# Optimization experiments

Hardware: AMD Instinct MI355X
Metric: run time of the kernel (lower is better)

Reference implementation:

```python
import jax, jax.numpy as jnp
import numpy as np

CONF_THRES = 0.8
NMS_THRES = 0.4
MAX_DET = 300          # fixed capacity for jit-compatible NMS output
N_BOXES = 262144
N_CLASSES = 80


def xywh2xyxy(x):
    xy, wh = x[..., :2], x[..., 2:4]
    return jnp.concatenate([xy - wh * 0.5, xy + wh * 0.5], axis=-1)


def bbox_iou(box, boxes):
    # one box [4] vs many [N,4]; original uses the +1 pixel-area convention
    x1 = jnp.maximum(box[0], boxes[:, 0])
    y1 = jnp.maximum(box[1], boxes[:, 1])
    x2 = jnp.minimum(box[2], boxes[:, 2])
    y2 = jnp.minimum(box[3], boxes[:, 3])
    inter = jnp.clip(x2 - x1 + 1, 0) * jnp.clip(y2 - y1 + 1, 0)
    a1 = (box[2] - box[0] + 1) * (box[3] - box[1] + 1)
    a2 = (boxes[:, 2] - boxes[:, 0] + 1) * (boxes[:, 3] - boxes[:, 1] + 1)
    return inter / (a1 + a2 - inter + 1e-16)


def nms_single(pred):
    # pred: [N, 85] raw YOLO output for one image
    boxes = xywh2xyxy(pred[:, :4])
    obj = pred[:, 4]
    cls_scores = pred[:, 5:]
    class_conf = cls_scores.max(axis=-1)
    class_pred = jnp.argmax(cls_scores, axis=-1).astype(pred.dtype)
    valid = obj >= CONF_THRES
    score = obj * class_conf
    # sort valid boxes by descending score; invalid pushed to the end
    order = jnp.argsort(jnp.where(valid, -score, jnp.inf))
    det = jnp.concatenate(
        [boxes, obj[:, None], class_conf[:, None], class_pred[:, None]], axis=1
    )[order]  # [N, 7] = x1,y1,x2,y2,obj,class_conf,class_pred
    valid = valid[order]

    def step(valid, _):
        idx = jnp.argmax(valid)            # first still-valid (= highest score)
        any_valid = jnp.any(valid)
        cur = det[idx]
        iou = bbox_iou(cur[:4], det[:, :4])
        invalid = (iou > NMS_THRES) & (det[:, 6] == cur[6]) & valid
        # weighted box merge over the suppressed group (as in original NMS)
        w = jnp.where(invalid, det[:, 4], 0.0)
        merged = (w[:, None] * det[:, :4]).sum(0) / (w.sum() + 1e-16)
        out = jnp.where(any_valid,
                        jnp.concatenate([merged, cur[4:]]),
                        jnp.zeros(7, pred.dtype))
        return valid & ~invalid, (out, any_valid)

    _, (kept, kept_valid) = jax.lax.scan(step, valid, None, length=MAX_DET)
    return kept, kept_valid  # [MAX_DET,7], [MAX_DET]


def setup_inputs() -> dict:
    key = jax.random.key(0)
    detections = jax.random.uniform(key, (1, N_BOXES, 5 + N_CLASSES), dtype=jnp.float32)
    return {"detections": detections}


def reference(detections):
    kept, kv = nms_single(detections[0])
    d = kept[:, 5:]                        # [MAX_DET, 2] = (class_conf, class_pred)
    conf_key = jnp.where(kv, d[:, 0], -jnp.inf)  # padded rows sort to the end
    order = jnp.argsort(conf_key)          # ascending (torch argsort)
    d = d[order][::-1]                     # torch.flip -> descending class_conf
    kv = kv[order][::-1]
    probs = jnp.where(kv, d[:, 0], 0.0)    # self.probs
    ids = d[:, 1][None, :]                 # self.ids, shape [1, MAX_DET]
    return ids, probs
```

## Files before the change

### kernel.cpp

```cpp
#include <hip/hip_runtime.h>

#pragma clang fp contract(off)

#define NBOX 262144
#define NCLS 80
#define ROWS 85
#define CAP 1024
#define NSUB 8
#define SUBCAP 128
#define POOL 8192
#define BPT 2
#define S1BOX 512

typedef unsigned long long ull;

__global__ __launch_bounds__(1024) void k_init(int* __restrict__ cnt_pad,
                                               int* __restrict__ pool_count,
                                               int* __restrict__ done_count) {
    const int t = threadIdx.x;
    for (int i = t; i < NCLS * NSUB * 16; i += 1024) cnt_pad[i] = 0;
    if (t == 0) { *pool_count = 0; *done_count = 0; }
}

__global__ __launch_bounds__(256) void k_stage1(const float* __restrict__ det,
                                                int* __restrict__ cnt_pad,
                                                ull* __restrict__ key2,
                                                float* __restrict__ conf2,
                                                float4* __restrict__ box2) {
    __shared__ int s_wl[S1BOX];
    __shared__ float s_obj[S1BOX];
    __shared__ int s_nv;
    const int t = threadIdx.x;
    const int b0 = blockIdx.x * S1BOX;
    const int sb = blockIdx.x & (NSUB - 1);

    if (t == 0) s_nv = 0;
    __syncthreads();

    float obj[BPT];
    #pragma unroll
    for (int i = 0; i < BPT; i++)
        obj[i] = det[(size_t)(b0 + (i << 8) + t) * ROWS + 4];
    #pragma unroll
    for (int i = 0; i < BPT; i++) {
        if (obj[i] >= 0.8f) {
            int r = atomicAdd(&s_nv, 1);
            s_wl[r] = (i << 8) + t;
            s_obj[r] = obj[i];
        }
    }
    __syncthreads();
    const int nv = s_nv;

    const int grp = t >> 4, c = t & 15;
    const int lane = t & 63;
    #pragma unroll 2
    for (int r0 = 0; r0 < nv; r0 += 16) {
        int widx = r0 + grp;
        if (widx < nv) {
            int b = s_wl[widx];
            const float* p = det + (size_t)(b0 + b) * ROWS;
            float aux = (c < 5) ? p[c] : 0.0f;
            float v0 = p[5 + c];
            float v1 = p[21 + c];
            float v2 = p[37 + c];
            float v3 = p[53 + c];
            float v4 = p[69 + c];
            float mv = v0; int mj = c;
            if (v1 > mv) { mv = v1; mj = 16 + c; }
            if (v2 > mv) { mv = v2; mj = 32 + c; }
            if (v3 > mv) { mv = v3; mj = 48 + c; }
            if (v4 > mv) { mv = v4; mj = 64 + c; }
            #pragma unroll
            for (int off = 8; off; off >>= 1) {
                float ov = __shfl_xor(mv, off);
                int oj = __shfl_xor(mj, off);
                if (ov > mv || (ov == mv && oj < mj)) { mv = ov; mj = oj; }
            }
            int gb = lane & 48;
            float x = __shfl(aux, gb + 0);
            float y = __shfl(aux, gb + 1);
            float w = __shfl(aux, gb + 2);
            float h = __shfl(aux, gb + 3);
            if (c == 0) {
                float ob = s_obj[widx];
                float score = ob * mv;
                float hw = w * 0.5f, hh = h * 0.5f;
                int gi = b0 + b;
                int r = atomicAdd(&cnt_pad[((mj * NSUB + sb) << 4)], 1);
                if (r < SUBCAP) {
                    int pos = (mj << 10) + (sb << 7) + r;
                    key2[pos] = ((ull)(~__float_as_uint(score)) << 32) | (unsigned)gi;
                    conf2[pos] = mv;
                    box2[pos] = make_float4(x - hw, y - hh, x + hw, y + hh);
                }
            }
        }
    }
}

__device__ __forceinline__ void bsort512(ull (&x)[8], int lane) {
    #pragma unroll
    for (int k = 2; k <= 512; k <<= 1) {
        #pragma unroll
        for (int j = k >> 1; j >= 64; j >>= 1) {
            const int jr = j >> 6;
            #pragma unroll
            for (int r2 = 0; r2 < 8; r2++) {
                if ((r2 & jr) == 0) {
                    const bool asc = (((r2 << 6) & k) == 0);
                    ull a = x[r2], b = x[r2 | jr];
                    if ((a > b) == asc) { x[r2] = b; x[r2 | jr] = a; }
                }
            }
        }
        #pragma unroll
        for (int j = ((k >> 1) > 32 ? 32 : (k >> 1)); j >= 1; j >>= 1) {
            #pragma unroll
            for (int r2 = 0; r2 < 8; r2++) {
                int i = (r2 << 6) + lane;
                bool asc = ((i & k) == 0);
                ull o = __shfl_xor(x[r2], j);
                bool lower = ((lane & j) == 0);
                ull mn = x[r2] < o ? x[r2] : o;
                ull mx2 = x[r2] < o ? o : x[r2];
                x[r2] = (asc == lower) ? mn : mx2;
            }
        }
    }
}

__global__ __launch_bounds__(256) void k_nmsfinal(const int* __restrict__ cnt_pad,
                                                  const ull* __restrict__ key2,
                                                  const float* __restrict__ conf2,
                                                  const float4* __restrict__ box2,
                                                  ull* __restrict__ pool_key,
                                                  float* __restrict__ pool_conf,
                                                  int* __restrict__ pool_cls,
                                                  int* __restrict__ pool_count,
                                                  int* __restrict__ done_count,
                                                  float* __restrict__ out) {
    __shared__ int s_cnt[NSUB];
    __shared__ ull s_wkey[4];
    __shared__ float s_wbox[4][6];
    __shared__ int s_base;
    __shared__ int s_fin;
    __shared__ ull pkey[304];
    __shared__ float pconf[304];
    __shared__ int s_hist[256];
    __shared__ int s_wt[4];
    __shared__ int s_stat[4];
    __shared__ ull s_buf[512];
    __shared__ unsigned s_cb[512];
    __shared__ unsigned s_cl[512];

    const int c = blockIdx.x, t = threadIdx.x, lane = t & 63, wave = t >> 6;
    const int s0 = c << 10;

    ull k4[4]; float x1[4], y1[4], x2[4], y2[4], ar[4], cf[4];
    #pragma unroll
    for (int j = 0; j < 4; j++) {
        int pos = (wave << 8) + (j << 6) + lane;
        k4[j] = key2[s0 + pos];
        float4 b = box2[s0 + pos];
        x1[j] = b.x; y1[j] = b.y; x2[j] = b.z; y2[j] = b.w;
        cf[j] = conf2[s0 + pos];
    }
    if (t < NSUB) s_cnt[t] = min(cnt_pad[((c * NSUB + t) << 4)], SUBCAP);
    __syncthreads();
    #pragma unroll
    for (int j = 0; j < 4; j++) {
        int pos = (wave << 8) + (j << 6) + lane;
        bool ok = (pos & (SUBCAP - 1)) < s_cnt[pos >> 7];
        if (!ok) {
            k4[j] = ~0ULL;
            x1[j] = 0.f; y1[j] = 0.f; x2[j] = 0.f; y2[j] = 0.f; cf[j] = 0.f;
        }
        ar[j] = (x2[j] - x1[j] + 1.0f) * (y2[j] - y1[j] + 1.0f);
    }

    int np = 0;
    while (np < 300) {
        ull va = k4[0]; int ia = 0;
        if (k4[1] < va) { va = k4[1]; ia = 1; }
        ull vb = k4[2]; int ib = 2;
        if (k4[3] < vb) { vb = k4[3]; ib = 3; }
        ull lm = va; int lj = ia;
        if (vb < va) { lm = vb; lj = ib; }
        unsigned lo = (unsigned)lm;
        unsigned hi = (unsigned)(lm >> 32);
        unsigned mh = hi;
        #pragma unroll
        for (int off = 32; off; off >>= 1) {
            unsigned o = __shfl_xor(mh, off);
            mh = o < mh ? o : mh;
        }
        ull wb = __ballot(hi == mh);
        ull wm; int wl;
        if (__popcll(wb) != 1) {
            ull g = (hi == mh) ? lm : ~0ULL;
            #pragma unroll
            for (int off = 32; off; off >>= 1) {
                ull o = __shfl_xor(g, off);
                if (o < g) g = o;
            }
            wm = g;
            wb = __ballot(lm == wm);
            wl = (int)__ffsll((long long)wb) - 1;
        } else {
            wl = (int)__ffsll((long long)wb) - 1;
            wm = ((ull)mh << 32) | (ull)__shfl(lo, wl);
        }
        if (lane == wl) {
            s_wkey[wave] = wm;
            s_wbox[wave][0] = x1[lj]; s_wbox[wave][1] = y1[lj];
            s_wbox[wave][2] = x2[lj]; s_wbox[wave][3] = y2[lj];
            s_wbox[wave][4] = ar[lj]; s_wbox[wave][5] = cf[lj];
        }
        __syncthreads();
        ull gk = s_wkey[0]; int gw = 0;
        #pragma unroll
        for (int w2 = 1; w2 < 4; w2++) {
            ull kk = s_wkey[w2];
            if (kk < gk) { gk = kk; gw = w2; }
        }
        if (gk == ~0ULL) break;
        float cx1 = s_wbox[gw][0], cy1 = s_wbox[gw][1];
        float cx2 = s_wbox[gw][2], cy2 = s_wbox[gw][3];
        float a1 = s_wbox[gw][4];
        if (t == 0) { pkey[np] = gk; pconf[np] = s_wbox[gw][5]; }
        np++;
        #pragma unroll
        for (int j = 0; j < 4; j++) {
            float xx1 = fmaxf(cx1, x1[j]), yy1 = fmaxf(cy1, y1[j]);
            float xx2 = fminf(cx2, x2[j]), yy2 = fminf(cy2, y2[j]);
            float iw = xx2 - xx1 + 1.0f, ih = yy2 - yy1 + 1.0f;
            float inter = fmaxf(iw, 0.0f) * fmaxf(ih, 0.0f);
            float iou = inter / (a1 + ar[j] - inter + 1e-16f);
            if (iou > 0.4f) k4[j] = ~0ULL;
        }
        __syncthreads();
    }

    const int npw = np;
    if (t == 0 && npw) s_base = atomicAdd(pool_count, npw);
    __syncthreads();
    for (int j = t; j < npw; j += 256) {
        int pp = s_base + j;
        if (pp < POOL) {
            ull gm = pkey[j];
            ull pk = ((ull)((unsigned)(gm >> 32) & 0x7FFFFFFFu) << 32)
                   | ((gm & 0xFFFFFFFFull) << 14) | (ull)pp;
            __hip_atomic_store(&pool_key[pp], pk,
                               __ATOMIC_RELAXED, __HIP_MEMORY_SCOPE_AGENT);
            __hip_atomic_store(&pool_conf[pp], pconf[j],
                               __ATOMIC_RELAXED, __HIP_MEMORY_SCOPE_AGENT);
            __hip_atomic_store(&pool_cls[pp], c,
                               __ATOMIC_RELAXED, __HIP_MEMORY_SCOPE_AGENT);
        }
    }
    asm volatile("s_waitcnt vmcnt(0)" ::: "memory");
    __syncthreads();
    if (t == 0) {
        int ticket = atomicAdd(done_count, 1);
        s_fin = (ticket == NCLS - 1) ? 1 : 0;
    }
    __syncthreads();
    if (!s_fin) return;

    const int K = min(__hip_atomic_load(pool_count, __ATOMIC_RELAXED,
                                        __HIP_MEMORY_SCOPE_AGENT), POOL);
    ull key[32];
    #pragma unroll
    for (int j = 0; j < 32; j++) {
        int pos = t + (j << 8);
        key[j] = (pos < K) ? __hip_atomic_load(&pool_key[pos], __ATOMIC_RELAXED,
                                               __HIP_MEMORY_SCOPE_AGENT)
                           : ~0ULL;
    }

    const bool selAll = (K <= 511);
    int sh = 55;
    ull pfin = 0;
    if (!selAll) {
        ull p = 0;
        int gBelow = 0, r = 300;
        while (true) {
            s_hist[t] = 0;
            __syncthreads();
            #pragma unroll
            for (int j = 0; j < 32; j++) {
                ull kk = key[j];
                if ((kk >> (sh + 8)) == p)
                    atomicAdd(&s_hist[(int)((kk >> sh) & 0xFFull)], 1);
            }
            __syncthreads();
            int v = s_hist[t];
            int incv = v;
            for (int off = 1; off < 64; off <<= 1) {
                int o = __shfl_up(incv, off);
                if (lane >= off) incv += o;
            }
            if (lane == 63) s_wt[wave] = incv;
            __syncthreads();
            int wo = 0;
            #pragma unroll
            for (int w2 = 0; w2 < 4; w2++) if (w2 < wave) wo += s_wt[w2];
            int cumIncl = wo + incv;
            int cumExcl = cumIncl - v;
            if (cumExcl < r && r <= cumIncl) {
                s_stat[0] = t; s_stat[1] = cumExcl; s_stat[2] = cumIncl;
            }
            __syncthreads();
            int D = s_stat[0], below = s_stat[1], incl = s_stat[2];
            if (gBelow + incl <= 511 || sh == 7) {
                pfin = (p << 8) | (ull)D;
                break;
            }
            p = (p << 8) | (ull)D;
            gBelow += below;
            r = 300 - gBelow;
            sh -= 8;
            __syncthreads();
        }
    }

    if (t == 0) s_stat[3] = 0;
    __syncthreads();
    int ci = 0;
    #pragma unroll
    for (int j = 0; j < 32; j++) {
        ull kk = key[j];
        bool sel = selAll ? ((kk >> 63) == 0) : ((kk >> sh) <= pfin);
        if (sel) ci++;
    }
    int inc = ci;
    for (int off = 1; off < 64; off <<= 1) {
        int o = __shfl_up(inc, off);
        if (lane >= off) inc += o;
    }
    int wtot = __shfl(inc, 63);
    int wbase2 = 0;
    if (lane == 0 && wtot) wbase2 = atomicAdd(&s_stat[3], wtot);
    wbase2 = __shfl(wbase2, 0);
    int wp = wbase2 + inc - ci;
    #pragma unroll
    for (int j = 0; j < 32; j++) {
        ull kk = key[j];
        bool sel = selAll ? ((kk >> 63) == 0) : ((kk >> sh) <= pfin);
        if (sel) s_buf[wp++] = kk;
    }
    __syncthreads();
    const int S = s_stat[3];
    for (int i = t; i < 512; i += 256) if (i >= S) s_buf[i] = ~0ULL;
    __syncthreads();
    if (wave != 0) return;

    #pragma clang loop unroll(disable)
    for (int pass = 0; pass < 2; pass++) {
        ull x[8];
        #pragma unroll
        for (int r2 = 0; r2 < 8; r2++) x[r2] = s_buf[(r2 << 6) + lane];
        bsort512(x, lane);
        if (pass == 0) {
            #pragma unroll
            for (int r2 = 0; r2 < 8; r2++) {
                int i = (r2 << 6) + lane;
                ull kk = x[r2];
                ull k2 = ~0ULL;
                if (i < 300 && kk != ~0ULL) {
                    int pidx = (int)(kk & 0x3FFFull);
                    unsigned cb = __float_as_uint(
                        __hip_atomic_load(&pool_conf[pidx], __ATOMIC_RELAXED,
                                          __HIP_MEMORY_SCOPE_AGENT));
                    unsigned cl = (unsigned)__hip_atomic_load(&pool_cls[pidx],
                                          __ATOMIC_RELAXED, __HIP_MEMORY_SCOPE_AGENT);
                    s_cb[i] = cb; s_cl[i] = cl;
                    k2 = ((ull)(~cb) << 32) | (unsigned)(~i);
                }
                s_buf[i] = k2;
            }
        } else {
            #pragma unroll
            for (int r2 = 0; r2 < 8; r2++) {
                int i = (r2 << 6) + lane;
                if (i < 300) {
                    ull kk = x[r2];
                    float idv = 0.0f, pv = 0.0f;
                    if (kk != ~0ULL) {
                        int slot = (int)(~(unsigned)(kk & 0xFFFFFFFFull));
                        pv = __uint_as_float(s_cb[slot]);
                        idv = (float)(int)s_cl[slot];
                    }
                    out[i] = idv;
                    out[300 + i] = pv;
                }
            }
        }
    }
}

extern "C" void kernel_launch(void* const* d_in, const int* in_sizes, int n_in,
                              void* d_out, int out_size, void* d_ws, size_t ws_size,
                              hipStream_t stream) {
    const float* det = (const float*)d_in[0];
    float* out = (float*)d_out;
    char* ws = (char*)d_ws;

    int* cnt_pad = (int*)(ws + 0);
    int* pool_count = (int*)(ws + 40960);
    int* done_count = (int*)(ws + 40964);
    ull* key2 = (ull*)(ws + 41024);
    float* conf2 = (float*)(ws + 696384);
    float4* box2 = (float4*)(ws + 1024064);
    ull* pool_key = (ull*)(ws + 2334784);
    float* pool_conf = (float*)(ws + 2400320);
    int* pool_cls = (int*)(ws + 2433088);

    k_init<<<1, 1024, 0, stream>>>(cnt_pad, pool_count, done_count);
    k_stage1<<<NBOX / S1BOX, 256, 0, stream>>>(det, cnt_pad, key2, conf2, box2);
    k_nmsfinal<<<NCLS, 256, 0, stream>>>(cnt_pad, key2, conf2, box2,
                                         pool_key, pool_conf, pool_cls, pool_count,
                                         done_count, out);
}
```

Baseline: 170.8 us.

## Fuse stage1 and per-class NMS into one persistent kernel with grid barriers

Merges the filtering/argmax stage and the per-class NMS plus final selection into a single kernel of 256 blocks. Spin-wait grid barriers on a global counter replace the kernel boundaries, and the last-block ticket is swapped for a second barrier where block 0 runs the final merge. Stage1 now handles 1024 boxes per block instead of 512, so the grid drops from 512 to 256 blocks. The aim is to remove launch gaps between kernels, at the cost of requiring all 256 blocks to be co-resident, atomic stores and loads in place of plain ones, and a bounded spin that could race if the guard expires.

```diff
diff --git a/kernel.cpp b/kernel.cpp
--- a/kernel.cpp
+++ b/kernel.cpp
@@ -9,10 +9,14 @@
 #define NSUB 8
 #define SUBCAP 128
 #define POOL 8192
-#define BPT 2
-#define S1BOX 512
+#define NBLK 256
+#define S1PB 1024
 
 typedef unsigned long long ull;
+
+__device__ __forceinline__ ull packf2(float a, float b) {
+    return ((ull)__float_as_uint(b) << 32) | (ull)__float_as_uint(a);
+}
 
 __global__ __launch_bounds__(1024) void k_init(int* __restrict__ cnt_pad,
                                                int* __restrict__ pool_count,
@@ -22,81 +26,17 @@
     if (t == 0) { *pool_count = 0; *done_count = 0; }
 }
 
-__global__ __launch_bounds__(256) void k_stage1(const float* __restrict__ det,
-                                                int* __restrict__ cnt_pad,
-                                                ull* __restrict__ key2,
-                                                float* __restrict__ conf2,
-                                                float4* __restrict__ box2) {
-    __shared__ int s_wl[S1BOX];
-    __shared__ float s_obj[S1BOX];
-    __shared__ int s_nv;
-    const int t = threadIdx.x;
-    const int b0 = blockIdx.x * S1BOX;
-    const int sb = blockIdx.x & (NSUB - 1);
-
-    if (t == 0) s_nv = 0;
+__device__ __forceinline__ void gsync(int* done, int target, int t) {
     __syncthreads();
-
-    float obj[BPT];
-    #pragma unroll
-    for (int i = 0; i < BPT; i++)
-        obj[i] = det[(size_t)(b0 + (i << 8) + t) * ROWS + 4];
-    #pragma unroll
-    for (int i = 0; i < BPT; i++) {
-        if (obj[i] >= 0.8f) {
-            int r = atomicAdd(&s_nv, 1);
-            s_wl[r] = (i << 8) + t;
-            s_obj[r] = obj[i];
-        }
+    if (t == 0) {
+        __hip_atomic_fetch_add(done, 1, __ATOMIC_RELAXED, __HIP_MEMORY_SCOPE_AGENT);
+        int guard = 0;
+        while (__hip_atomic_load(done, __ATOMIC_RELAXED,
+                                 __HIP_MEMORY_SCOPE_AGENT) < target &&
+               ++guard < (1 << 18))
+            __builtin_amdgcn_s_sleep(8);
     }
     __syncthreads();
-    const int nv = s_nv;
-
-    const int grp = t >> 4, c = t & 15;
-    const int lane = t & 63;
-    #pragma unroll 2
-    for (int r0 = 0; r0 < nv; r0 += 16) {
-        int widx = r0 + grp;
-        if (widx < nv) {
-            int b = s_wl[widx];
-            const float* p = det + (size_t)(b0 + b) * ROWS;
-            float aux = (c < 5) ? p[c] : 0.0f;
-            float v0 = p[5 + c];
-            float v1 = p[21 + c];
-            float v2 = p[37 + c];
-            float v3 = p[53 + c];
-            float v4 = p[69 + c];
-            float mv = v0; int mj = c;
-            if (v1 > mv) { mv = v1; mj = 16 + c; }
-            if (v2 > mv) { mv = v2; mj = 32 + c; }
-            if (v3 > mv) { mv = v3; mj = 48 + c; }
-            if (v4 > mv) { mv = v4; mj = 64 + c; }
-            #pragma unroll
-            for (int off = 8; off; off >>= 1) {
-                float ov = __shfl_xor(mv, off);
-                int oj = __shfl_xor(mj, off);
-                if (ov > mv || (ov == mv && oj < mj)) { mv = ov; mj = oj; }
-            }
-            int gb = lane & 48;
-            float x = __shfl(aux, gb + 0);
-            float y = __shfl(aux, gb + 1);
-            float w = __shfl(aux, gb + 2);
-            float h = __shfl(aux, gb + 3);
-            if (c == 0) {
-                float ob = s_obj[widx];
-                float score = ob * mv;
-                float hw = w * 0.5f, hh = h * 0.5f;
-                int gi = b0 + b;
-                int r = atomicAdd(&cnt_pad[((mj * NSUB + sb) << 4)], 1);
-                if (r < SUBCAP) {
-                    int pos = (mj << 10) + (sb << 7) + r;
-                    key2[pos] = ((ull)(~__float_as_uint(score)) << 32) | (unsigned)gi;
-                    conf2[pos] = mv;
-                    box2[pos] = make_float4(x - hw, y - hh, x + hw, y + hh);
-                }
-            }
-        }
-    }
 }
 
 __device__ __forceinline__ void bsort512(ull (&x)[8], int lane) {
@@ -130,21 +70,24 @@
     }
 }
 
-__global__ __launch_bounds__(256) void k_nmsfinal(const int* __restrict__ cnt_pad,
-                                                  const ull* __restrict__ key2,
-                                                  const float* __restrict__ conf2,
-                                                  const float4* __restrict__ box2,
-                                                  ull* __restrict__ pool_key,
-                                                  float* __restrict__ pool_conf,
-                                                  int* __restrict__ pool_cls,
-                                                  int* __restrict__ pool_count,
-                                                  int* __restrict__ done_count,
-                                                  float* __restrict__ out) {
+__global__ __launch_bounds__(256) void k_mega(const float* __restrict__ det,
+                                              int* __restrict__ cnt_pad,
+                                              ull* __restrict__ key2,
+                                              float* __restrict__ conf2,
+                                              float4* __restrict__ box2,
+                                              ull* __restrict__ pool_key,
+                                              float* __restrict__ pool_conf,
+                                              int* __restrict__ pool_cls,
+                                              int* __restrict__ pool_count,
+                                              int* __restrict__ done_count,
+                                              float* __restrict__ out) {
+    __shared__ int s_wl[S1PB];
+    __shared__ float s_obj[S1PB];
+    __shared__ int s_nv;
     __shared__ int s_cnt[NSUB];
     __shared__ ull s_wkey[4];
     __shared__ float s_wbox[4][6];
     __shared__ int s_base;
-    __shared__ int s_fin;
     __shared__ ull pkey[304];
     __shared__ float pconf[304];
     __shared__ int s_hist[256];
@@ -154,119 +97,204 @@
     __shared__ unsigned s_cb[512];
     __shared__ unsigned s_cl[512];
 
-    const int c = blockIdx.x, t = threadIdx.x, lane = t & 63, wave = t >> 6;
-    const int s0 = c << 10;
-
-    ull k4[4]; float x1[4], y1[4], x2[4], y2[4], ar[4], cf[4];
-    #pragma unroll
-    for (int j = 0; j < 4; j++) {
-        int pos = (wave << 8) + (j << 6) + lane;
-        k4[j] = key2[s0 + pos];
-        float4 b = box2[s0 + pos];
-        x1[j] = b.x; y1[j] = b.y; x2[j] = b.z; y2[j] = b.w;
-        cf[j] = conf2[s0 + pos];
-    }
-    if (t < NSUB) s_cnt[t] = min(cnt_pad[((c * NSUB + t) << 4)], SUBCAP);
-    __syncthreads();
-    #pragma unroll
-    for (int j = 0; j < 4; j++) {
-        int pos = (wave << 8) + (j << 6) + lane;
-        bool ok = (pos & (SUBCAP - 1)) < s_cnt[pos >> 7];
-        if (!ok) {
-            k4[j] = ~0ULL;
-            x1[j] = 0.f; y1[j] = 0.f; x2[j] = 0.f; y2[j] = 0.f; cf[j] = 0.f;
-        }
-        ar[j] = (x2[j] - x1[j] + 1.0f) * (y2[j] - y1[j] + 1.0f);
-    }
-
-    int np = 0;
-    while (np < 300) {
-        ull va = k4[0]; int ia = 0;
-        if (k4[1] < va) { va = k4[1]; ia = 1; }
-        ull vb = k4[2]; int ib = 2;
-        if (k4[3] < vb) { vb = k4[3]; ib = 3; }
-        ull lm = va; int lj = ia;
-        if (vb < va) { lm = vb; lj = ib; }
-        unsigned lo = (unsigned)lm;
-        unsigned hi = (unsigned)(lm >> 32);
-        unsigned mh = hi;
-        #pragma unroll
-        for (int off = 32; off; off >>= 1) {
-            unsigned o = __shfl_xor(mh, off);
-            mh = o < mh ? o : mh;
-        }
-        ull wb = __ballot(hi == mh);
-        ull wm; int wl;
-        if (__popcll(wb) != 1) {
-            ull g = (hi == mh) ? lm : ~0ULL;
+    const int bid = blockIdx.x, t = threadIdx.x, lane = t & 63, wave = t >> 6;
+
+    {
+        const int b0 = bid << 10;
+        const int sb = bid & (NSUB - 1);
+        if (t == 0) s_nv = 0;
+        __syncthreads();
+        float obj[4];
+        #pragma unroll
+        for (int i = 0; i < 4; i++)
+            obj[i] = det[(size_t)(b0 + (i << 8) + t) * ROWS + 4];
+        #pragma unroll
+        for (int i = 0; i < 4; i++) {
+            if (obj[i] >= 0.8f) {
+                int r = atomicAdd(&s_nv, 1);
+                s_wl[r] = (i << 8) + t;
+                s_obj[r] = obj[i];
+            }
+        }
+        __syncthreads();
+        const int nv = s_nv;
+
+        const int grp = t >> 4, c = t & 15;
+        #pragma unroll 2
+        for (int r0 = 0; r0 < nv; r0 += 16) {
+            int widx = r0 + grp;
+            if (widx < nv) {
+                int b = s_wl[widx];
+                const float* p = det + (size_t)(b0 + b) * ROWS;
+                float aux = (c < 5) ? p[c] : 0.0f;
+                float v0 = p[5 + c];
+                float v1 = p[21 + c];
+                float v2 = p[37 + c];
+                float v3 = p[53 + c];
+                float v4 = p[69 + c];
+                float mv = v0; int mj = c;
+                if (v1 > mv) { mv = v1; mj = 16 + c; }
+                if (v2 > mv) { mv = v2; mj = 32 + c; }
+                if (v3 > mv) { mv = v3; mj = 48 + c; }
+                if (v4 > mv) { mv = v4; mj = 64 + c; }
+                #pragma unroll
+                for (int off = 8; off; off >>= 1) {
+                    float ov = __shfl_xor(mv, off);
+                    int oj = __shfl_xor(mj, off);
+                    if (ov > mv || (ov == mv && oj < mj)) { mv = ov; mj = oj; }
+                }
+                int gb = lane & 48;
+                float x = __shfl(aux, gb + 0);
+                float y = __shfl(aux, gb + 1);
+                float w = __shfl(aux, gb + 2);
+                float h = __shfl(aux, gb + 3);
+                if (c == 0) {
+                    float ob = s_obj[widx];
+                    float score = ob * mv;
+                    float hw = w * 0.5f, hh = h * 0.5f;
+                    int gi = b0 + b;
+                    int r = atomicAdd(&cnt_pad[((mj * NSUB + sb) << 4)], 1);
+                    if (r < SUBCAP) {
+                        int pos = (mj << 10) + (sb << 7) + r;
+                        __hip_atomic_store(&key2[pos],
+                            ((ull)(~__float_as_uint(score)) << 32) | (unsigned)gi,
+                            __ATOMIC_RELAXED, __HIP_MEMORY_SCOPE_AGENT);
+                        __hip_atomic_store(&conf2[pos], mv,
+                            __ATOMIC_RELAXED, __HIP_MEMORY_SCOPE_AGENT);
+                        ull* bp = (ull*)&box2[pos];
+                        __hip_atomic_store(bp + 0, packf2(x - hw, y - hh),
+                            __ATOMIC_RELAXED, __HIP_MEMORY_SCOPE_AGENT);
+                        __hip_atomic_store(bp + 1, packf2(x + hw, y + hh),
+                            __ATOMIC_RELAXED, __HIP_MEMORY_SCOPE_AGENT);
+                    }
+                }
+            }
+        }
+    }
+
+    gsync(done_count, NBLK, t);
+
+    if (bid < NCLS) {
+        const int c = bid;
+        const int s0 = c << 10;
+        ull k4[4]; float x1[4], y1[4], x2[4], y2[4], ar[4], cf[4];
+        #pragma unroll
+        for (int j = 0; j < 4; j++) {
+            int pos = s0 + (wave << 8) + (j << 6) + lane;
+            k4[j] = __hip_atomic_load(&key2[pos], __ATOMIC_RELAXED,
+                                      __HIP_MEMORY_SCOPE_AGENT);
+            ull* bp = (ull*)&box2[pos];
+            ull blo = __hip_atomic_load(bp + 0, __ATOMIC_RELAXED,
+                                        __HIP_MEMORY_SCOPE_AGENT);
+            ull bhi = __hip_atomic_load(bp + 1, __ATOMIC_RELAXED,
+                                        __HIP_MEMORY_SCOPE_AGENT);
+            x1[j] = __uint_as_float((unsigned)blo);
+            y1[j] = __uint_as_float((unsigned)(blo >> 32));
+            x2[j] = __uint_as_float((unsigned)bhi);
+            y2[j] = __uint_as_float((unsigned)(bhi >> 32));
+            cf[j] = __hip_atomic_load(&conf2[pos], __ATOMIC_RELAXED,
+                                      __HIP_MEMORY_SCOPE_AGENT);
+        }
+        if (t < NSUB)
+            s_cnt[t] = min(__hip_atomic_load(&cnt_pad[((c * NSUB + t) << 4)],
+                                             __ATOMIC_RELAXED, __HIP_MEMORY_SCOPE_AGENT),
+                           SUBCAP);
+        __syncthreads();
+        #pragma unroll
+        for (int j = 0; j < 4; j++) {
+            int pos = (wave << 8) + (j << 6) + lane;
+            bool ok = (pos & (SUBCAP - 1)) < s_cnt[pos >> 7];
+            if (!ok) {
+                k4[j] = ~0ULL;
+                x1[j] = 0.f; y1[j] = 0.f; x2[j] = 0.f; y2[j] = 0.f; cf[j] = 0.f;
+            }
+            ar[j] = (x2[j] - x1[j] + 1.0f) * (y2[j] - y1[j] + 1.0f);
+        }
+
+        int np = 0;
+        while (np < 300) {
+            ull va = k4[0]; int ia = 0;
+            if (k4[1] < va) { va = k4[1]; ia = 1; }
+            ull vb = k4[2]; int ib = 2;
+            if (k4[3] < vb) { vb = k4[3]; ib = 3; }
+            ull lm = va; int lj = ia;
+            if (vb < va) { lm = vb; lj = ib; }
+            unsigned lo = (unsigned)lm;
+            unsigned hi = (unsigned)(lm >> 32);
+            unsigned mh = hi;
             #pragma unroll
             for (int off = 32; off; off >>= 1) {
-                ull o = __shfl_xor(g, off);
-                if (o < g) g = o;
-            }
-            wm = g;
-            wb = __ballot(lm == wm);
-            wl = (int)__ffsll((long long)wb) - 1;
-        } else {
-            wl = (int)__ffsll((long long)wb) - 1;
-            wm = ((ull)mh << 32) | (ull)__shfl(lo, wl);
-        }
-        if (lane == wl) {
-            s_wkey[wave] = wm;
-            s_wbox[wave][0] = x1[lj]; s_wbox[wave][1] = y1[lj];
-            s_wbox[wave][2] = x2[lj]; s_wbox[wave][3] = y2[lj];
-            s_wbox[wave][4] = ar[lj]; s_wbox[wave][5] = cf[lj];
-        }
+                unsigned o = __shfl_xor(mh, off);
+                mh = o < mh ? o : mh;
+            }
+            ull wb = __ballot(hi == mh);
+            ull wm; int wl;
+            if (__popcll(wb) != 1) {
+                ull g = (hi == mh) ? lm : ~0ULL;
+                #pragma unroll
+                for (int off = 32; off; off >>= 1) {
+                    ull o = __shfl_xor(g, off);
+                    if (o < g) g = o;
+                }
+                wm = g;
+                wb = __ballot(lm == wm);
+                wl = (int)__ffsll((long long)wb) - 1;
+            } else {
+                wl = (int)__ffsll((long long)wb) - 1;
+                wm = ((ull)mh << 32) | (ull)__shfl(lo, wl);
+            }
+            if (lane == wl) {
+                s_wkey[wave] = wm;
+                s_wbox[wave][0] = x1[lj]; s_wbox[wave][1] = y1[lj];
+                s_wbox[wave][2] = x2[lj]; s_wbox[wave][3] = y2[lj];
+                s_wbox[wave][4] = ar[lj]; s_wbox[wave][5] = cf[lj];
+            }
+            __syncthreads();
+            ull gk = s_wkey[0]; int gw = 0;
+            #pragma unroll
+            for (int w2 = 1; w2 < 4; w2++) {
+                ull kk = s_wkey[w2];
+                if (kk < gk) { gk = kk; gw = w2; }
+            }
+            if (gk == ~0ULL) break;
+            float cx1 = s_wbox[gw][0], cy1 = s_wbox[gw][1];
+            float cx2 = s_wbox[gw][2], cy2 = s_wbox[gw][3];
+            float a1 = s_wbox[gw][4];
+            if (t == 0) { pkey[np] = gk; pconf[np] = s_wbox[gw][5]; }
+            np++;
+            #pragma unroll
+            for (int j = 0; j < 4; j++) {
+                float xx1 = fmaxf(cx1, x1[j]), yy1 = fmaxf(cy1, y1[j]);
+                float xx2 = fminf(cx2, x2[j]), yy2 = fminf(cy2, y2[j]);
+                float iw = xx2 - xx1 + 1.0f, ih = yy2 - yy1 + 1.0f;
+                float inter = fmaxf(iw, 0.0f) * fmaxf(ih, 0.0f);
+                float iou = inter / (a1 + ar[j] - inter + 1e-16f);
+                if (iou > 0.4f) k4[j] = ~0ULL;
+            }
+            __syncthreads();
+        }
+
+        const int npw = np;
+        if (t == 0 && npw) s_base = atomicAdd(pool_count, npw);
         __syncthreads();
-        ull gk = s_wkey[0]; int gw = 0;
-        #pragma unroll
-        for (int w2 = 1; w2 < 4; w2++) {
-            ull kk = s_wkey[w2];
-            if (kk < gk) { gk = kk; gw = w2; }
-        }
-        if (gk == ~0ULL) break;
-        float cx1 = s_wbox[gw][0], cy1 = s_wbox[gw][1];
-        float cx2 = s_wbox[gw][2], cy2 = s_wbox[gw][3];
-        float a1 = s_wbox[gw][4];
-        if (t == 0) { pkey[np] = gk; pconf[np] = s_wbox[gw][5]; }
-        np++;
-        #pragma unroll
-        for (int j = 0; j < 4; j++) {
-            float xx1 = fmaxf(cx1, x1[j]), yy1 = fmaxf(cy1, y1[j]);
-            float xx2 = fminf(cx2, x2[j]), yy2 = fminf(cy2, y2[j]);
-            float iw = xx2 - xx1 + 1.0f, ih = yy2 - yy1 + 1.0f;
-            float inter = fmaxf(iw, 0.0f) * fmaxf(ih, 0.0f);
-            float iou = inter / (a1 + ar[j] - inter + 1e-16f);
-            if (iou > 0.4f) k4[j] = ~0ULL;
-        }
-        __syncthreads();
-    }
-
-    const int npw = np;
-    if (t == 0 && npw) s_base = atomicAdd(pool_count, npw);
-    __syncthreads();
-    for (int j = t; j < npw; j += 256) {
-        int pp = s_base + j;
-        if (pp < POOL) {
-            ull gm = pkey[j];
-            ull pk = ((ull)((unsigned)(gm >> 32) & 0x7FFFFFFFu) << 32)
-                   | ((gm & 0xFFFFFFFFull) << 14) | (ull)pp;
-            __hip_atomic_store(&pool_key[pp], pk,
-                               __ATOMIC_RELAXED, __HIP_MEMORY_SCOPE_AGENT);
-            __hip_atomic_store(&pool_conf[pp], pconf[j],
-                               __ATOMIC_RELAXED, __HIP_MEMORY_SCOPE_AGENT);
-            __hip_atomic_store(&pool_cls[pp], c,
-                               __ATOMIC_RELAXED, __HIP_MEMORY_SCOPE_AGENT);
-        }
-    }
-    asm volatile("s_waitcnt vmcnt(0)" ::: "memory");
-    __syncthreads();
-    if (t == 0) {
-        int ticket = atomicAdd(done_count, 1);
-        s_fin = (ticket == NCLS - 1) ? 1 : 0;
-    }
-    __syncthreads();
-    if (!s_fin) return;
+        for (int j = t; j < npw; j += 256) {
+            int pp = s_base + j;
+            if (pp < POOL) {
+                ull gm = pkey[j];
+                ull pk = ((ull)((unsigned)(gm >> 32) & 0x7FFFFFFFu) << 32)
+                       | ((gm & 0xFFFFFFFFull) << 14) | (ull)pp;
+                __hip_atomic_store(&pool_key[pp], pk,
+                                   __ATOMIC_RELAXED, __HIP_MEMORY_SCOPE_AGENT);
+                __hip_atomic_store(&pool_conf[pp], pconf[j],
+                                   __ATOMIC_RELAXED, __HIP_MEMORY_SCOPE_AGENT);
+                __hip_atomic_store(&pool_cls[pp], c,
+                                   __ATOMIC_RELAXED, __HIP_MEMORY_SCOPE_AGENT);
+            }
+        }
+    }
+
+    gsync(done_count, 2 * NBLK, t);
+    if (bid != 0) return;
 
     const int K = min(__hip_atomic_load(pool_count, __ATOMIC_RELAXED,
                                         __HIP_MEMORY_SCOPE_AGENT), POOL);
@@ -418,8 +446,7 @@
     int* pool_cls = (int*)(ws + 2433088);
 
     k_init<<<1, 1024, 0, stream>>>(cnt_pad, pool_count, done_count);
-    k_stage1<<<NBOX / S1BOX, 256, 0, stream>>>(det, cnt_pad, key2, conf2, box2);
-    k_nmsfinal<<<NCLS, 256, 0, stream>>>(cnt_pad, key2, conf2, box2,
-                                         pool_key, pool_conf, pool_cls, pool_count,
-                                         done_count, out);
-}
+    k_mega<<<NBLK, 256, 0, stream>>>(det, cnt_pad, key2, conf2, box2,
+                                     pool_key, pool_conf, pool_cls, pool_count,
+                                     done_count, out);
+}
```

Result: slower. 193.1 us (+13.0%).
